# Kernel tuning notes

Measured on AMD Instinct MI355X. Metric: run time of the kernel, lower is better.

Reference implementation:

```python
import jax, jax.numpy as jnp
import numpy as np

# dims: S spaces, B batch, T tokens, D = dense_dim = concept_dim, K codebook size
S, B, T, D, K = 8, 8, 2048, 64, 512
BN_EPS = 1e-3  # keras BatchNormalization default


def setup_inputs() -> dict:
    key = jax.random.key(0)
    k0, k1, k2 = jax.random.split(key, 3)
    x = jax.random.normal(k0, (B, T, D), jnp.float32)
    W = jax.random.normal(k1, (S, D, D), jnp.float32) * 0.1   # per-space Dense kernels
    b = jnp.zeros((S, D), jnp.float32)                         # per-space Dense biases
    gamma = jnp.ones((S, D), jnp.float32)                      # BN scale
    beta = jnp.zeros((S, D), jnp.float32)                      # BN shift
    bn_mean = jnp.zeros((S, D), jnp.float32)                   # BN moving mean
    bn_var = jnp.ones((S, D), jnp.float32)                     # BN moving var
    E = jax.random.normal(k2, (S, K, D), jnp.float32)          # per-space codebooks
    return dict(x=x, W=W, b=b, gamma=gamma, beta=beta,
                bn_mean=bn_mean, bn_var=bn_var, E=E)


def reference(x, W, b, gamma, beta, bn_mean, bn_var, E):
    # per-space projection: Dense -> BatchNorm (inference) -> softmax gate
    proj = jnp.einsum('btd,sde->sbte', x, W) + b[:, None, None, :]          # [S,B,T,D]
    inv = jax.lax.rsqrt(bn_var + BN_EPS)
    bn = gamma[:, None, None, :] * (proj - bn_mean[:, None, None, :]) * inv[:, None, None, :] \
         + beta[:, None, None, :]
    att = jax.nn.softmax(bn, axis=-1)
    z = x[None] * att                                                       # z_e_att, [S,B,T,D]

    # squared euclidean distance to each code; argmin(norm) == argmin(dist^2)
    d2 = (jnp.sum(z * z, axis=-1, keepdims=True)
          - 2.0 * jnp.einsum('sbtc,skc->sbtk', z, E)
          + jnp.sum(E * E, axis=-1)[:, None, None, :])                      # [S,B,T,K]
    z_k = jnp.argmin(d2, axis=-1)                                           # [S,B,T] int

    # gather nearest codes per space, then add_n over spaces (set_att != 0)
    z_q_s = E[jnp.arange(S)[:, None, None], z_k]                            # [S,B,T,D]
    z_q = jnp.sum(z_q_s, axis=0)                                            # [B,T,D]
    z_e = jnp.sum(z, axis=0)                                                # [B,T,D]
    z_k = z_k.astype(jnp.int64) if z_k.dtype != jnp.int64 else z_k          # tf.argmin -> int64
    return z_q, z_e, z_k
```

## Files before the change

kernel.cpp:

```cpp
#include <hip/hip_runtime.h>
#include <cfloat>
#include <cmath>

#define SN 8
#define DN 64
#define KN 512
#define NN 16384
#define CK 64
#define REPAIR_THR 2e-3f
#define GAP_IK 8u
#define MAXFLAG 65536

#define WS_CNT 0
#define WS_SCL 16
#define WS_OFF (16 + SN*DN)
#define WS_E2  (WS_OFF + SN*DN)
#define WS_ENT (WS_E2 + SN*KN)
#define WS_WTH (WS_ENT + MAXFLAG)
#define WS_WTL (WS_WTH + SN*64*32)
#define WS_EH  (WS_WTL + SN*64*32)
#define WS_EL  (WS_EH + SN*KN*32)
#define WS_ZP  (WS_EL + SN*KN*32)
#define WS_END (WS_ZP + SN*NN*DN)

#define LDS_ZH 0
#define LDS_ZL 8192
#define LDS_EH 16384
#define LDS_EL 24576
#define LDS_TOTAL 32768

#define FB_LDS_R2    17408
#define FB_LDS_TAIL  33792
#define FB_LDS_TOTAL 34816

typedef __attribute__((ext_vector_type(8))) short bf16x8;
typedef __attribute__((ext_vector_type(4))) short s16x4;
typedef __attribute__((ext_vector_type(4))) float f32x4;

__device__ inline short bf_hi(float f, float& rem) {
    unsigned u = __float_as_uint(f);
    unsigned r = (u + 0x7fffu + ((u >> 16) & 1u)) & 0xffff0000u;
    rem = f - __uint_as_float(r);
    return (short)(r >> 16);
}
__device__ inline short bf_rn(float f) {
    unsigned u = __float_as_uint(f);
    return (short)((u + 0x7fffu + ((u >> 16) & 1u)) >> 16);
}
__device__ inline void cvt4(float a, float b, float c, float d, s16x4& h, s16x4& l) {
    float r0, r1, r2, r3;
    h.x = bf_hi(a, r0); h.y = bf_hi(b, r1); h.z = bf_hi(c, r2); h.w = bf_hi(d, r3);
    l.x = bf_rn(r0); l.y = bf_rn(r1); l.z = bf_rn(r2); l.w = bf_rn(r3);
}

union U8 { bf16x8 v; s16x4 q[2]; };

__global__ void prep_kernel(const float* __restrict__ b, const float* __restrict__ gamma,
                            const float* __restrict__ beta, const float* __restrict__ bmean,
                            const float* __restrict__ bvar, const float* __restrict__ E,
                            float* __restrict__ ws) {
    int tid = blockIdx.x * 256 + threadIdx.x;
    if (tid < SN * KN) {
        const float* er = E + (size_t)tid * DN;
        double a = 0.0;
        for (int d = 0; d < DN; ++d) { double v = (double)er[d]; a = fma(v, v, a); }
        ws[WS_E2 + tid] = (float)a;
    }
    int u = tid - SN * KN;
    if (u >= 0 && u < SN * DN) {
        double inv = 1.0 / sqrt((double)bvar[u] + 0.001);
        double sc  = (double)gamma[u] * inv;
        ws[WS_SCL + u] = (float)sc;
        ws[WS_OFF + u] = (float)(((double)b[u] - (double)bmean[u]) * sc + (double)beta[u]);
    }
}

__global__ void prep2_kernel(const float* __restrict__ E, float* __restrict__ ws) {
    int idx = blockIdx.x * 256 + threadIdx.x;
    int sk = idx >> 4, c4 = idx & 15;
    int k = sk & (KN - 1);
    float4 g = ((const float4*)E)[(size_t)sk * 16 + c4];
    s16x4 h4, l4;
    cvt4(g.x, g.y, g.z, g.w, h4, l4);
    size_t off = ((size_t)sk * 128 + c4 * 8) ^ ((k & 7) << 4);
    *(s16x4*)((char*)(ws + WS_EH) + off) = h4;
    *(s16x4*)((char*)(ws + WS_EL) + off) = l4;
}

__global__ void prep2w_kernel(const float* __restrict__ W, float* __restrict__ ws) {
    __shared__ float wt[64][65];
    int s = blockIdx.x;
    int tid = threadIdx.x;
    #pragma unroll
    for (int r = 0; r < 4; ++r) {
        int i = r * 256 + tid;
        float4 g = ((const float4*)W)[(size_t)s * 1024 + i];
        int d = i >> 4, c4 = i & 15;
        wt[d][c4 * 4 + 0] = g.x; wt[d][c4 * 4 + 1] = g.y;
        wt[d][c4 * 4 + 2] = g.z; wt[d][c4 * 4 + 3] = g.w;
    }
    __syncthreads();
    #pragma unroll
    for (int r = 0; r < 4; ++r) {
        int j = r * 256 + tid;
        int e = j >> 4, c4 = j & 15;
        s16x4 h4, l4;
        cvt4(wt[c4 * 4 + 0][e], wt[c4 * 4 + 1][e], wt[c4 * 4 + 2][e], wt[c4 * 4 + 3][e], h4, l4);
        size_t off = (size_t)(s * 64 + e) * 128 + c4 * 8;
        *(s16x4*)((char*)(ws + WS_WTH) + off) = h4;
        *(s16x4*)((char*)(ws + WS_WTL) + off) = l4;
    }
}

__launch_bounds__(256, 4)
__global__ void main_kernel(const float* __restrict__ x, float* __restrict__ ws,
                            float* __restrict__ out, int entcap) {
    extern __shared__ char smraw[];
    const int tid = threadIdx.x;
    const int s  = blockIdx.y;
    const int n0 = blockIdx.x * 64;
    const int lane = tid & 63;
    const int w    = tid >> 6;
    const int cc   = lane & 15;
    const int kq   = lane >> 4;
    const int arow = w * 16 + cc;
    const int axor = (arow & 7) << 4;

    const char* eimg_h = (const char*)(ws + WS_EH) + (size_t)s * KN * 128;
    const char* eimg_l = (const char*)(ws + WS_EL) + (size_t)s * KN * 128;

    float4 pf0 = *(const float4*)(eimg_h + tid * 16);
    float4 pf1 = *(const float4*)(eimg_h + 4096 + tid * 16);
    float4 pf2 = *(const float4*)(eimg_l + tid * 16);
    float4 pf3 = *(const float4*)(eimg_l + 4096 + tid * 16);

    U8 xah[2], xal[2];
    #pragma unroll
    for (int ks = 0; ks < 2; ++ks) {
        const float* xr = x + (size_t)(n0 + arow) * DN + ks * 32 + kq * 8;
        float4 a = *(const float4*)xr;
        float4 b2 = *(const float4*)(xr + 4);
        s16x4 h0, l0, h1, l1;
        cvt4(a.x, a.y, a.z, a.w, h0, l0);
        cvt4(b2.x, b2.y, b2.z, b2.w, h1, l1);
        xah[ks].q[0] = h0; xah[ks].q[1] = h1;
        xal[ks].q[0] = l0; xal[ks].q[1] = l1;
    }

    const char* wimg_h = (const char*)(ws + WS_WTH) + (size_t)s * 64 * 128;
    const char* wimg_l = (const char*)(ws + WS_WTL) + (size_t)s * 64 * 128;
    f32x4 pa[4];
    #pragma unroll
    for (int nt = 0; nt < 4; ++nt) pa[nt] = (f32x4){0.f, 0.f, 0.f, 0.f};
    #pragma unroll
    for (int ks = 0; ks < 2; ++ks) {
        #pragma unroll
        for (int nt = 0; nt < 4; ++nt) {
            int brow = nt * 16 + cc;
            bf16x8 bh = *(const bf16x8*)(wimg_h + brow * 128 + ks * 64 + kq * 16);
            bf16x8 bl = *(const bf16x8*)(wimg_l + brow * 128 + ks * 64 + kq * 16);
            pa[nt] = __builtin_amdgcn_mfma_f32_16x16x32_bf16(xah[ks].v, bh, pa[nt], 0, 0, 0);
            pa[nt] = __builtin_amdgcn_mfma_f32_16x16x32_bf16(xah[ks].v, bl, pa[nt], 0, 0, 0);
            pa[nt] = __builtin_amdgcn_mfma_f32_16x16x32_bf16(xal[ks].v, bh, pa[nt], 0, 0, 0);
        }
    }

    float sclv[4], oflv[4];
    #pragma unroll
    for (int nt = 0; nt < 4; ++nt) {
        sclv[nt] = ws[WS_SCL + s * 64 + nt * 16 + cc];
        oflv[nt] = ws[WS_OFF + s * 64 + nt * 16 + cc];
    }
    float zzq[4];
    #pragma unroll
    for (int r = 0; r < 4; ++r) {
        int t = w * 16 + kq * 4 + r;
        float v0 = fmaf(pa[0][r], sclv[0], oflv[0]);
        float v1 = fmaf(pa[1][r], sclv[1], oflv[1]);
        float v2 = fmaf(pa[2][r], sclv[2], oflv[2]);
        float v3 = fmaf(pa[3][r], sclv[3], oflv[3]);
        float mx = fmaxf(fmaxf(v0, v1), fmaxf(v2, v3));
        mx = fmaxf(mx, __shfl_xor(mx, 1)); mx = fmaxf(mx, __shfl_xor(mx, 2));
        mx = fmaxf(mx, __shfl_xor(mx, 4)); mx = fmaxf(mx, __shfl_xor(mx, 8));
        float e0 = expf(v0 - mx), e1 = expf(v1 - mx), e2v = expf(v2 - mx), e3 = expf(v3 - mx);
        float sm = e0 + e1 + e2v + e3;
        sm += __shfl_xor(sm, 1); sm += __shfl_xor(sm, 2);
        sm += __shfl_xor(sm, 4); sm += __shfl_xor(sm, 8);
        float inv = 1.0f / sm;
        float att[4] = { e0 * inv, e1 * inv, e2v * inv, e3 * inv };
        float zz = 0.f;
        int txor = (t & 7) << 4;
        #pragma unroll
        for (int nt = 0; nt < 4; ++nt) {
            int e = nt * 16 + cc;
            float xv = x[(size_t)(n0 + t) * DN + e];
            float z = xv * att[nt];
            zz += z * z;
            float rem; short zh = bf_hi(z, rem); short zl = bf_rn(rem);
            int zoff = (t * 128 + e * 2) ^ txor;
            *(short*)(smraw + LDS_ZH + zoff) = zh;
            *(short*)(smraw + LDS_ZL + zoff) = zl;
            ws[WS_ZP + ((size_t)s * NN + n0 + t) * DN + e] = z;
        }
        zz += __shfl_xor(zz, 1); zz += __shfl_xor(zz, 2);
        zz += __shfl_xor(zz, 4); zz += __shfl_xor(zz, 8);
        zzq[r] = (zz + 16.f) * 4096.f;
    }
    *(float4*)(smraw + LDS_EH + tid * 16) = pf0;
    *(float4*)(smraw + LDS_EH + 4096 + tid * 16) = pf1;
    *(float4*)(smraw + LDS_EL + tid * 16) = pf2;
    *(float4*)(smraw + LDS_EL + 4096 + tid * 16) = pf3;
    __syncthreads();

    unsigned m1[4], m2[4];
    #pragma unroll
    for (int r = 0; r < 4; ++r) { m1[r] = 0xFFFFFFFFu; m2[r] = 0xFFFFFFFFu; }

    for (int kk = 0; kk < KN; kk += CK) {
        if (kk + CK < KN) {
            const char* nbh = eimg_h + (size_t)(kk + CK) * 128;
            const char* nbl = eimg_l + (size_t)(kk + CK) * 128;
            pf0 = *(const float4*)(nbh + tid * 16);
            pf1 = *(const float4*)(nbh + 4096 + tid * 16);
            pf2 = *(const float4*)(nbl + tid * 16);
            pf3 = *(const float4*)(nbl + 4096 + tid * 16);
        }
        float e2v[4];
        #pragma unroll
        for (int nt = 0; nt < 4; ++nt) e2v[nt] = ws[WS_E2 + s * KN + kk + nt * 16 + cc];

        bf16x8 zah[2], zal[2];
        #pragma unroll
        for (int ks = 0; ks < 2; ++ks) {
            int aoff = (arow * 128 + kq * 16 + ks * 64) ^ axor;
            zah[ks] = *(const bf16x8*)(smraw + LDS_ZH + aoff);
            zal[ks] = *(const bf16x8*)(smraw + LDS_ZL + aoff);
        }
        f32x4 acc[4];
        #pragma unroll
        for (int nt = 0; nt < 4; ++nt) acc[nt] = (f32x4){0.f, 0.f, 0.f, 0.f};
        #pragma unroll
        for (int ks = 0; ks < 2; ++ks) {
            #pragma unroll
            for (int nt = 0; nt < 4; ++nt) {
                int brow = nt * 16 + cc;
                int boff = (brow * 128 + kq * 16 + ks * 64) ^ ((brow & 7) << 4);
                bf16x8 bh = *(const bf16x8*)(smraw + LDS_EH + boff);
                bf16x8 bl = *(const bf16x8*)(smraw + LDS_EL + boff);
                acc[nt] = __builtin_amdgcn_mfma_f32_16x16x32_bf16(zah[ks], bh, acc[nt], 0, 0, 0);
                acc[nt] = __builtin_amdgcn_mfma_f32_16x16x32_bf16(zah[ks], bl, acc[nt], 0, 0, 0);
                acc[nt] = __builtin_amdgcn_mfma_f32_16x16x32_bf16(zal[ks], bh, acc[nt], 0, 0, 0);
            }
        }
        #pragma unroll
        for (int nt = 0; nt < 4; ++nt) {
            unsigned kx = (unsigned)(kk + nt * 16 + cc);
            float eb = fmaf(4096.f, e2v[nt], 0.f);
            #pragma unroll
            for (int r = 0; r < 4; ++r) {
                float cell = fmaf(-8192.f, acc[nt][r], zzq[r] + eb);
                float dc = fminf(cell, 4194300.f);
                unsigned key = (((unsigned)dc) << 9) | kx;
                m2[r] = min(m2[r], max(m1[r], key));
                m1[r] = min(m1[r], key);
            }
        }
        if (kk + CK < KN) {
            __syncthreads();
            *(float4*)(smraw + LDS_EH + tid * 16) = pf0;
            *(float4*)(smraw + LDS_EH + 4096 + tid * 16) = pf1;
            *(float4*)(smraw + LDS_EL + tid * 16) = pf2;
            *(float4*)(smraw + LDS_EL + 4096 + tid * 16) = pf3;
            __syncthreads();
        }
    }

    #pragma unroll
    for (int mask = 1; mask <= 8; mask <<= 1) {
        #pragma unroll
        for (int r = 0; r < 4; ++r) {
            unsigned o1 = (unsigned)__shfl_xor((int)m1[r], mask);
            unsigned o2 = (unsigned)__shfl_xor((int)m2[r], mask);
            unsigned hi = max(m1[r], o1);
            m1[r] = min(m1[r], o1);
            m2[r] = min(min(m2[r], o2), hi);
        }
    }
    #pragma unroll
    for (int r = 0; r < 4; ++r) {
        int n = n0 + w * 16 + kq * 4 + r;
        if (cc == 0) {
            int k1 = (int)(m1[r] & 511u);
            out[2 * NN * DN + s * NN + n] = (float)k1;
            if ((m2[r] >> 9) - (m1[r] >> 9) <= GAP_IK) {
                int idx = atomicAdd((int*)ws, 1);
                if (idx < entcap) ((int*)ws)[WS_ENT + idx] = (s << 14) | n;
            }
        }
    }
}

__launch_bounds__(256, 4)
__global__ void main_fb_kernel(const float* __restrict__ x, const float* __restrict__ W,
                               const float* __restrict__ E, float* __restrict__ ws,
                               float* __restrict__ out, int entcap) {
    extern __shared__ char smraw[];
    float4* xs4 = (float4*)smraw;
    float4* ws4 = (float4*)(smraw + FB_LDS_R2);
    char* ehb = smraw;
    char* elb = smraw + 8192;
    char* zhb = smraw + FB_LDS_R2;
    char* zlb = smraw + FB_LDS_R2 + 8192;
    float* tailf = (float*)(smraw + FB_LDS_TAIL);
    float* e2s = tailf; float* scl = tailf + 64; float* ofl = tailf + 128; float* zzs = tailf + 192;

    const int tid = threadIdx.x;
    const int tg = tid >> 4, lg = tid & 15;
    const int s  = blockIdx.y;
    const int n0 = blockIdx.x * 64;
    const float4* xg4 = (const float4*)x;
    const float4* Wg4 = (const float4*)W;
    const float4* Eg4 = (const float4*)E;

    #pragma unroll
    for (int r = 0; r < 4; ++r) {
        int i = r * 256 + tid;
        xs4[(i >> 4) * 17 + (i & 15)] = xg4[n0 * 16 + i];
        ws4[i] = Wg4[s * 1024 + i];
    }
    if (tid < 64) { scl[tid] = ws[WS_SCL + s * 64 + tid]; ofl[tid] = ws[WS_OFF + s * 64 + tid]; }
    __syncthreads();

    float pa[4][4];
    #pragma unroll
    for (int ti = 0; ti < 4; ++ti)
        #pragma unroll
        for (int j = 0; j < 4; ++j) pa[ti][j] = 0.f;
    #pragma unroll 4
    for (int c = 0; c < 16; ++c) {
        float4 xv[4], wv[4];
        #pragma unroll
        for (int ti = 0; ti < 4; ++ti) xv[ti] = xs4[(tg * 4 + ti) * 17 + c];
        #pragma unroll
        for (int dd = 0; dd < 4; ++dd) wv[dd] = ws4[(c * 4 + dd) * 16 + lg];
        #pragma unroll
        for (int ti = 0; ti < 4; ++ti) {
            float a0 = pa[ti][0], a1 = pa[ti][1], a2 = pa[ti][2], a3 = pa[ti][3];
            a0 = fmaf(xv[ti].x, wv[0].x, a0); a0 = fmaf(xv[ti].y, wv[1].x, a0);
            a0 = fmaf(xv[ti].z, wv[2].x, a0); a0 = fmaf(xv[ti].w, wv[3].x, a0);
            a1 = fmaf(xv[ti].x, wv[0].y, a1); a1 = fmaf(xv[ti].y, wv[1].y, a1);
            a1 = fmaf(xv[ti].z, wv[2].y, a1); a1 = fmaf(xv[ti].w, wv[3].y, a1);
            a2 = fmaf(xv[ti].x, wv[0].z, a2); a2 = fmaf(xv[ti].y, wv[1].z, a2);
            a2 = fmaf(xv[ti].z, wv[2].z, a2); a2 = fmaf(xv[ti].w, wv[3].z, a2);
            a3 = fmaf(xv[ti].x, wv[0].w, a3); a3 = fmaf(xv[ti].y, wv[1].w, a3);
            a3 = fmaf(xv[ti].z, wv[2].w, a3); a3 = fmaf(xv[ti].w, wv[3].w, a3);
            pa[ti][0] = a0; pa[ti][1] = a1; pa[ti][2] = a2; pa[ti][3] = a3;
        }
    }
    __syncthreads();

    {
        float s0 = scl[lg * 4 + 0], s1 = scl[lg * 4 + 1], s2 = scl[lg * 4 + 2], s3 = scl[lg * 4 + 3];
        float o0 = ofl[lg * 4 + 0], o1 = ofl[lg * 4 + 1], o2 = ofl[lg * 4 + 2], o3 = ofl[lg * 4 + 3];
        #pragma unroll
        for (int ti = 0; ti < 4; ++ti) {
            int t = tg * 4 + ti;
            float v0 = fmaf(pa[ti][0], s0, o0);
            float v1 = fmaf(pa[ti][1], s1, o1);
            float v2 = fmaf(pa[ti][2], s2, o2);
            float v3 = fmaf(pa[ti][3], s3, o3);
            float mx = fmaxf(fmaxf(v0, v1), fmaxf(v2, v3));
            mx = fmaxf(mx, __shfl_xor(mx, 1)); mx = fmaxf(mx, __shfl_xor(mx, 2));
            mx = fmaxf(mx, __shfl_xor(mx, 4)); mx = fmaxf(mx, __shfl_xor(mx, 8));
            float e0 = expf(v0 - mx), e1 = expf(v1 - mx), e2v = expf(v2 - mx), e3 = expf(v3 - mx);
            float sm = e0 + e1 + e2v + e3;
            sm += __shfl_xor(sm, 1); sm += __shfl_xor(sm, 2);
            sm += __shfl_xor(sm, 4); sm += __shfl_xor(sm, 8);
            float inv = 1.0f / sm;
            float4 xv = xs4[t * 17 + lg];
            float z0 = xv.x * (e0 * inv), z1 = xv.y * (e1 * inv);
            float z2 = xv.z * (e2v * inv), z3 = xv.w * (e3 * inv);
            float zz = z0 * z0 + z1 * z1 + z2 * z2 + z3 * z3;
            zz += __shfl_xor(zz, 1); zz += __shfl_xor(zz, 2);
            zz += __shfl_xor(zz, 4); zz += __shfl_xor(zz, 8);
            if (lg == 0) zzs[t] = zz;
            s16x4 h4, l4;
            cvt4(z0, z1, z2, z3, h4, l4);
            int zoff = (t * 128 + lg * 8) ^ ((t & 7) << 4);
            *(s16x4*)(zhb + zoff) = h4;
            *(s16x4*)(zlb + zoff) = l4;
            float* pz = out + NN * DN + (size_t)(n0 + t) * DN + lg * 4;
            atomicAdd(pz + 0, z0); atomicAdd(pz + 1, z1);
            atomicAdd(pz + 2, z2); atomicAdd(pz + 3, z3);
        }
    }
    __syncthreads();

    const int lane = tid & 63;
    const int w    = tid >> 6;
    const int arow = w * 16 + (lane & 15);
    const int kg16 = (lane >> 4) * 16;
    const int axor = (arow & 7) << 4;
    const int abase = arow * 128 + kg16;

    float zzv[4];
    #pragma unroll
    for (int r = 0; r < 4; ++r) zzv[r] = zzs[w * 16 + (lane >> 4) * 4 + r];

    float m1[4], m2[4]; int k1[4];
    #pragma unroll
    for (int r = 0; r < 4; ++r) { m1[r] = FLT_MAX; m2[r] = FLT_MAX; k1[r] = 0x7fffffff; }

    for (int kk = 0; kk < KN; kk += CK) {
        __syncthreads();
        #pragma unroll
        for (int r = 0; r < 4; ++r) {
            int i = r * 256 + tid;
            float4 g = Eg4[(s * KN + kk) * 16 + i];
            int row = i >> 4, c4 = i & 15;
            s16x4 h4, l4;
            cvt4(g.x, g.y, g.z, g.w, h4, l4);
            int off = (row * 128 + c4 * 8) ^ ((row & 7) << 4);
            *(s16x4*)(ehb + off) = h4;
            *(s16x4*)(elb + off) = l4;
        }
        if (tid < 64) e2s[tid] = ws[WS_E2 + s * KN + kk + tid];
        __syncthreads();

        f32x4 acc[4];
        #pragma unroll
        for (int nt = 0; nt < 4; ++nt) acc[nt] = (f32x4){0.f, 0.f, 0.f, 0.f};
        #pragma unroll
        for (int ks = 0; ks < 2; ++ks) {
            int aoff = (abase + ks * 64) ^ axor;
            bf16x8 ah = *(const bf16x8*)(zhb + aoff);
            bf16x8 al = *(const bf16x8*)(zlb + aoff);
            #pragma unroll
            for (int nt = 0; nt < 4; ++nt) {
                int brow = nt * 16 + (lane & 15);
                int boff = (brow * 128 + kg16 + ks * 64) ^ ((brow & 7) << 4);
                bf16x8 bh = *(const bf16x8*)(ehb + boff);
                bf16x8 bl = *(const bf16x8*)(elb + boff);
                acc[nt] = __builtin_amdgcn_mfma_f32_16x16x32_bf16(ah, bh, acc[nt], 0, 0, 0);
                acc[nt] = __builtin_amdgcn_mfma_f32_16x16x32_bf16(ah, bl, acc[nt], 0, 0, 0);
                acc[nt] = __builtin_amdgcn_mfma_f32_16x16x32_bf16(al, bh, acc[nt], 0, 0, 0);
            }
        }
        #pragma unroll
        for (int nt = 0; nt < 4; ++nt) {
            float e2v = e2s[nt * 16 + (lane & 15)];
            int kx = kk + nt * 16 + (lane & 15);
            #pragma unroll
            for (int r = 0; r < 4; ++r) {
                float d2 = fmaf(-2.0f, acc[nt][r], zzv[r]) + e2v;
                if (d2 < m1[r]) { m2[r] = m1[r]; m1[r] = d2; k1[r] = kx; }
                else if (d2 < m2[r]) { m2[r] = d2; }
            }
        }
    }

    #pragma unroll
    for (int mask = 1; mask <= 8; mask <<= 1) {
        #pragma unroll
        for (int r = 0; r < 4; ++r) {
            float om1 = __shfl_xor(m1[r], mask);
            int   ok1 = __shfl_xor(k1[r], mask);
            float om2 = __shfl_xor(m2[r], mask);
            bool better = (om1 < m1[r]) || (om1 == m1[r] && ok1 < k1[r]);
            float nm2 = better ? fminf(m1[r], om2) : fminf(om1, m2[r]);
            if (better) { m1[r] = om1; k1[r] = ok1; }
            m2[r] = nm2;
        }
    }
    #pragma unroll
    for (int r = 0; r < 4; ++r) {
        int t = w * 16 + (lane >> 4) * 4 + r;
        int n = n0 + t;
        if ((lane & 15) == 0) {
            out[2 * NN * DN + s * NN + n] = (float)k1[r];
            if (m2[r] - m1[r] < REPAIR_THR) {
                int idx = atomicAdd((int*)ws, 1);
                if (idx < entcap) ((int*)ws)[WS_ENT + idx] = (s << 14) | n;
            }
        }
        int kb = __shfl(k1[r], lane & 48);
        float4 eg = Eg4[(s * KN + kb) * 16 + (lane & 15)];
        float* q = out + (size_t)n * DN + (lane & 15) * 4;
        atomicAdd(q + 0, eg.x); atomicAdd(q + 1, eg.y);
        atomicAdd(q + 2, eg.z); atomicAdd(q + 3, eg.w);
    }
}

__global__ void reduce_kernel(const float* __restrict__ E, const float* __restrict__ ws,
                              float* __restrict__ out) {
    int idx = blockIdx.x * 256 + threadIdx.x;
    int n = idx >> 4, c = idx & 15;
    const float4* zp4 = (const float4*)(ws + WS_ZP);
    float4 ze = make_float4(0.f, 0.f, 0.f, 0.f);
    #pragma unroll
    for (int s = 0; s < SN; ++s) {
        float4 v = zp4[((size_t)s * NN + n) * 16 + c];
        ze.x += v.x; ze.y += v.y; ze.z += v.z; ze.w += v.w;
    }
    ((float4*)out)[NN * 16 + (size_t)n * 16 + c] = ze;

    float4 zq = make_float4(0.f, 0.f, 0.f, 0.f);
    #pragma unroll
    for (int s = 0; s < SN; ++s) {
        int k = (int)(out[2 * NN * DN + s * NN + n] + 0.5f);
        float4 e = ((const float4*)E)[((size_t)s * KN + k) * 16 + c];
        zq.x += e.x; zq.y += e.y; zq.z += e.z; zq.w += e.w;
    }
    ((float4*)out)[(size_t)n * 16 + c] = zq;
}

__global__ void repair_kernel(const float* __restrict__ x, const float* __restrict__ W,
                              const float* __restrict__ b, const float* __restrict__ gamma,
                              const float* __restrict__ beta, const float* __restrict__ bmean,
                              const float* __restrict__ bvar, const float* __restrict__ E,
                              float* __restrict__ ws, float* __restrict__ out, int entcap) {
    __shared__ double zd[64];
    __shared__ double red[256];
    __shared__ int redk[256];
    __shared__ double zzsh;
    __shared__ int shk[2];
    int cnt = ((int*)ws)[0]; if (cnt > entcap) cnt = entcap;
    const int tid = threadIdx.x;
    for (int idx = blockIdx.x; idx < cnt; idx += gridDim.x) {
        int code = ((int*)ws)[WS_ENT + idx];
        int s = code >> 14, n = code & (NN - 1);
        int e = tid & 63, q = tid >> 6;
        const float* xrow = x + (size_t)n * 64;
        double p0 = 0.0, p1 = 0.0, p2 = 0.0, p3 = 0.0;
        for (int d = q * 16; d < q * 16 + 16; d += 4) {
            p0 = fma((double)xrow[d],     (double)W[((size_t)s * 64 + d) * 64 + e],     p0);
            p1 = fma((double)xrow[d + 1], (double)W[((size_t)s * 64 + d + 1) * 64 + e], p1);
            p2 = fma((double)xrow[d + 2], (double)W[((size_t)s * 64 + d + 2) * 64 + e], p2);
            p3 = fma((double)xrow[d + 3], (double)W[((size_t)s * 64 + d + 3) * 64 + e], p3);
        }
        red[tid] = (p0 + p1) + (p2 + p3);
        __syncthreads();
        if (tid < 64) {
            double proj = (red[tid] + red[tid + 64]) + (red[tid + 128] + red[tid + 192]);
            double inv = 1.0 / sqrt((double)bvar[s * 64 + e] + 0.001);
            double bn = (double)gamma[s * 64 + e] * ((proj + (double)b[s * 64 + e]) - (double)bmean[s * 64 + e]) * inv
                      + (double)beta[s * 64 + e];
            double m = bn;
            #pragma unroll
            for (int mask = 1; mask <= 32; mask <<= 1) m = fmax(m, __shfl_xor(m, mask));
            double ex = exp(bn - m);
            double sm = ex;
            #pragma unroll
            for (int mask = 1; mask <= 32; mask <<= 1) sm += __shfl_xor(sm, mask);
            double z = (double)xrow[e] * (ex / sm);
            zd[e] = z;
            double zz = z * z;
            #pragma unroll
            for (int mask = 1; mask <= 32; mask <<= 1) zz += __shfl_xor(zz, mask);
            if (tid == 0) zzsh = zz;
        }
        __syncthreads();
        double bv = DBL_MAX; int bk = 1 << 30;
        for (int k = tid; k < KN; k += 256) {
            const float* er = E + ((size_t)s * KN + k) * 64;
            double d0 = 0.0, d1 = 0.0, d2a = 0.0, d3 = 0.0;
            double f0 = 0.0, f1 = 0.0, f2 = 0.0, f3 = 0.0;
            for (int d = 0; d < 64; d += 4) {
                double e0 = (double)er[d], e1 = (double)er[d + 1];
                double e2d = (double)er[d + 2], e3d = (double)er[d + 3];
                d0 = fma(zd[d], e0, d0);     d1 = fma(zd[d + 1], e1, d1);
                d2a = fma(zd[d + 2], e2d, d2a); d3 = fma(zd[d + 3], e3d, d3);
                f0 = fma(e0, e0, f0); f1 = fma(e1, e1, f1);
                f2 = fma(e2d, e2d, f2); f3 = fma(e3d, e3d, f3);
            }
            double dot = (d0 + d1) + (d2a + d3);
            double e2t = (f0 + f1) + (f2 + f3);
            double d2v = (zzsh - 2.0 * dot) + e2t;
            if (d2v < bv) { bv = d2v; bk = k; }
        }
        #pragma unroll
        for (int mask = 1; mask <= 32; mask <<= 1) {
            double ov = __shfl_xor(bv, mask);
            int   ok = __shfl_xor(bk, mask);
            if (ov < bv || (ov == bv && ok < bk)) { bv = ov; bk = ok; }
        }
        if ((tid & 63) == 0) { red[tid >> 6] = bv; redk[tid >> 6] = bk; }
        __syncthreads();
        if (tid == 0) {
            double m = red[0]; int mk = redk[0];
            for (int i = 1; i < 4; ++i)
                if (red[i] < m || (red[i] == m && redk[i] < mk)) { m = red[i]; mk = redk[i]; }
            int kold = (int)(out[2 * NN * 64 + s * NN + n] + 0.5f);
            shk[0] = mk; shk[1] = kold;
            out[2 * NN * 64 + s * NN + n] = (float)mk;
        }
        __syncthreads();
        int mk = shk[0], kold = shk[1];
        if (mk != kold && tid < 64)
            atomicAdd(out + n * 64 + tid, E[((size_t)s * KN + mk) * 64 + tid] - E[((size_t)s * KN + kold) * 64 + tid]);
        __syncthreads();
    }
}

extern "C" void kernel_launch(void* const* d_in, const int* in_sizes, int n_in,
                              void* d_out, int out_size, void* d_ws, size_t ws_size,
                              hipStream_t stream) {
    const float* x     = (const float*)d_in[0];
    const float* W     = (const float*)d_in[1];
    const float* b     = (const float*)d_in[2];
    const float* gamma = (const float*)d_in[3];
    const float* beta  = (const float*)d_in[4];
    const float* bmean = (const float*)d_in[5];
    const float* bvar  = (const float*)d_in[6];
    const float* E     = (const float*)d_in[7];
    float* out = (float*)d_out;
    float* ws  = (float*)d_ws;

    bool staged = ws_size >= (size_t)WS_END * 4;

    long avail = (long)(ws_size / 4) - WS_ENT - 16;
    if (avail < 0) avail = 0;
    int entcap = (int)(avail > MAXFLAG ? MAXFLAG : avail);
    if (staged) entcap = MAXFLAG;

    hipMemsetAsync(d_ws, 0, 64, stream);
    prep_kernel<<<18, 256, 0, stream>>>(b, gamma, beta, bmean, bvar, E, ws);
    dim3 grid(256, 8);
    if (staged) {
        prep2w_kernel<<<8, 256, 0, stream>>>(W, ws);
        prep2_kernel<<<256, 256, 0, stream>>>(E, ws);
        main_kernel<<<grid, 256, LDS_TOTAL, stream>>>(x, ws, out, entcap);
        reduce_kernel<<<1024, 256, 0, stream>>>(E, ws, out);
    } else {
        hipMemsetAsync(d_out, 0, (size_t)(2 * NN * DN) * sizeof(float), stream);
        main_fb_kernel<<<grid, 256, FB_LDS_TOTAL, stream>>>(x, W, E, ws, out, entcap);
    }
    repair_kernel<<<2048, 256, 0, stream>>>(x, W, b, gamma, beta, bmean, bvar, E, ws, out, entcap);
}
```

Before: 158.5 us.

## Merge prep kernels, double-buffer codebook LDS tiles, hoist z fragments

Folds the three preprocessing kernels into one launch and precomputes the scaled codebook norms so the inner loop does one fewer multiply. Double-buffers the codebook tiles in shared memory, which cuts the two barriers per chunk down to one. It also hoists the z-fragment LDS loads out of the loop, switches to fast exp, and drops the clamp on the distance key. The cost is more LDS per block (occupancy bound lowered from 4 to 3) and a smaller repair-flag capacity. The missing clamp and the fast exp could shift which argmin candidates get flagged for repair.

New measurement: 153.0 us. 3.5% less time.

```diff
diff --git a/kernel.cpp b/kernel.cpp
--- a/kernel.cpp
+++ b/kernel.cpp
@@ -9,7 +9,7 @@
 #define CK 64
 #define REPAIR_THR 2e-3f
 #define GAP_IK 8u
-#define MAXFLAG 65536
+#define MAXFLAG 32768
 
 #define WS_CNT 0
 #define WS_SCL 16
@@ -21,13 +21,13 @@
 #define WS_EH  (WS_WTL + SN*64*32)
 #define WS_EL  (WS_EH + SN*KN*32)
 #define WS_ZP  (WS_EL + SN*KN*32)
-#define WS_END (WS_ZP + SN*NN*DN)
+#define WS_E2S (WS_ZP + SN*NN*DN)
+#define WS_END (WS_E2S + SN*KN)
 
 #define LDS_ZH 0
 #define LDS_ZL 8192
-#define LDS_EH 16384
-#define LDS_EL 24576
-#define LDS_TOTAL 32768
+#define LDS_E0 16384
+#define LDS_TOTAL 49152
 
 #define FB_LDS_R2    17408
 #define FB_LDS_TAIL  33792
@@ -54,6 +54,62 @@
 }
 
 union U8 { bf16x8 v; s16x4 q[2]; };
+
+__global__ void prep_all_kernel(const float* __restrict__ b, const float* __restrict__ gamma,
+                                const float* __restrict__ beta, const float* __restrict__ bmean,
+                                const float* __restrict__ bvar, const float* __restrict__ W,
+                                const float* __restrict__ E, float* __restrict__ ws) {
+    __shared__ float wt[64][65];
+    const int blk = blockIdx.x, tid = threadIdx.x;
+    if (blk < 256) {
+        int idx = blk * 256 + tid;
+        int sk = idx >> 4, c4 = idx & 15;
+        int k = sk & (KN - 1);
+        float4 g = ((const float4*)E)[(size_t)sk * 16 + c4];
+        s16x4 h4, l4;
+        cvt4(g.x, g.y, g.z, g.w, h4, l4);
+        size_t off = ((size_t)sk * 128 + c4 * 8) ^ ((k & 7) << 4);
+        *(s16x4*)((char*)(ws + WS_EH) + off) = h4;
+        *(s16x4*)((char*)(ws + WS_EL) + off) = l4;
+    } else if (blk < 264) {
+        int s = blk - 256;
+        #pragma unroll
+        for (int r = 0; r < 4; ++r) {
+            int i = r * 256 + tid;
+            float4 g = ((const float4*)W)[(size_t)s * 1024 + i];
+            int d = i >> 4, c4 = i & 15;
+            wt[d][c4 * 4 + 0] = g.x; wt[d][c4 * 4 + 1] = g.y;
+            wt[d][c4 * 4 + 2] = g.z; wt[d][c4 * 4 + 3] = g.w;
+        }
+        __syncthreads();
+        #pragma unroll
+        for (int r = 0; r < 4; ++r) {
+            int j = r * 256 + tid;
+            int e = j >> 4, c4 = j & 15;
+            s16x4 h4, l4;
+            cvt4(wt[c4 * 4 + 0][e], wt[c4 * 4 + 1][e], wt[c4 * 4 + 2][e], wt[c4 * 4 + 3][e], h4, l4);
+            size_t off = (size_t)(s * 64 + e) * 128 + c4 * 8;
+            *(s16x4*)((char*)(ws + WS_WTH) + off) = h4;
+            *(s16x4*)((char*)(ws + WS_WTL) + off) = l4;
+        }
+    } else {
+        int t2 = (blk - 264) * 256 + tid;
+        if (t2 < SN * KN) {
+            const float* er = E + (size_t)t2 * DN;
+            double a = 0.0;
+            for (int d = 0; d < DN; ++d) { double v = (double)er[d]; a = fma(v, v, a); }
+            ws[WS_E2 + t2]  = (float)a;
+            ws[WS_E2S + t2] = (float)(a * 4096.0);
+        }
+        int u = t2 - SN * KN;
+        if (u >= 0 && u < SN * DN) {
+            double inv = 1.0 / sqrt((double)bvar[u] + 0.001);
+            double sc  = (double)gamma[u] * inv;
+            ws[WS_SCL + u] = (float)sc;
+            ws[WS_OFF + u] = (float)(((double)b[u] - (double)bmean[u]) * sc + (double)beta[u]);
+        }
+    }
+}
 
 __global__ void prep_kernel(const float* __restrict__ b, const float* __restrict__ gamma,
                             const float* __restrict__ beta, const float* __restrict__ bmean,
@@ -75,44 +131,7 @@
     }
 }
 
-__global__ void prep2_kernel(const float* __restrict__ E, float* __restrict__ ws) {
-    int idx = blockIdx.x * 256 + threadIdx.x;
-    int sk = idx >> 4, c4 = idx & 15;
-    int k = sk & (KN - 1);
-    float4 g = ((const float4*)E)[(size_t)sk * 16 + c4];
-    s16x4 h4, l4;
-    cvt4(g.x, g.y, g.z, g.w, h4, l4);
-    size_t off = ((size_t)sk * 128 + c4 * 8) ^ ((k & 7) << 4);
-    *(s16x4*)((char*)(ws + WS_EH) + off) = h4;
-    *(s16x4*)((char*)(ws + WS_EL) + off) = l4;
-}
-
-__global__ void prep2w_kernel(const float* __restrict__ W, float* __restrict__ ws) {
-    __shared__ float wt[64][65];
-    int s = blockIdx.x;
-    int tid = threadIdx.x;
-    #pragma unroll
-    for (int r = 0; r < 4; ++r) {
-        int i = r * 256 + tid;
-        float4 g = ((const float4*)W)[(size_t)s * 1024 + i];
-        int d = i >> 4, c4 = i & 15;
-        wt[d][c4 * 4 + 0] = g.x; wt[d][c4 * 4 + 1] = g.y;
-        wt[d][c4 * 4 + 2] = g.z; wt[d][c4 * 4 + 3] = g.w;
-    }
-    __syncthreads();
-    #pragma unroll
-    for (int r = 0; r < 4; ++r) {
-        int j = r * 256 + tid;
-        int e = j >> 4, c4 = j & 15;
-        s16x4 h4, l4;
-        cvt4(wt[c4 * 4 + 0][e], wt[c4 * 4 + 1][e], wt[c4 * 4 + 2][e], wt[c4 * 4 + 3][e], h4, l4);
-        size_t off = (size_t)(s * 64 + e) * 128 + c4 * 8;
-        *(s16x4*)((char*)(ws + WS_WTH) + off) = h4;
-        *(s16x4*)((char*)(ws + WS_WTL) + off) = l4;
-    }
-}
-
-__launch_bounds__(256, 4)
+__launch_bounds__(256, 3)
 __global__ void main_kernel(const float* __restrict__ x, float* __restrict__ ws,
                             float* __restrict__ out, int entcap) {
     extern __shared__ char smraw[];
@@ -182,7 +201,8 @@
         float mx = fmaxf(fmaxf(v0, v1), fmaxf(v2, v3));
         mx = fmaxf(mx, __shfl_xor(mx, 1)); mx = fmaxf(mx, __shfl_xor(mx, 2));
         mx = fmaxf(mx, __shfl_xor(mx, 4)); mx = fmaxf(mx, __shfl_xor(mx, 8));
-        float e0 = expf(v0 - mx), e1 = expf(v1 - mx), e2v = expf(v2 - mx), e3 = expf(v3 - mx);
+        float e0 = __expf(v0 - mx), e1 = __expf(v1 - mx);
+        float e2v = __expf(v2 - mx), e3 = __expf(v3 - mx);
         float sm = e0 + e1 + e2v + e3;
         sm += __shfl_xor(sm, 1); sm += __shfl_xor(sm, 2);
         sm += __shfl_xor(sm, 4); sm += __shfl_xor(sm, 8);
@@ -206,18 +226,31 @@
         zz += __shfl_xor(zz, 4); zz += __shfl_xor(zz, 8);
         zzq[r] = (zz + 16.f) * 4096.f;
     }
-    *(float4*)(smraw + LDS_EH + tid * 16) = pf0;
-    *(float4*)(smraw + LDS_EH + 4096 + tid * 16) = pf1;
-    *(float4*)(smraw + LDS_EL + tid * 16) = pf2;
-    *(float4*)(smraw + LDS_EL + 4096 + tid * 16) = pf3;
-    __syncthreads();
+
+    bf16x8 zah[2], zal[2];
+    #pragma unroll
+    for (int ks = 0; ks < 2; ++ks) {
+        int aoff = (arow * 128 + kq * 16 + ks * 64) ^ axor;
+        zah[ks] = *(const bf16x8*)(smraw + LDS_ZH + aoff);
+        zal[ks] = *(const bf16x8*)(smraw + LDS_ZL + aoff);
+    }
 
     unsigned m1[4], m2[4];
     #pragma unroll
     for (int r = 0; r < 4; ++r) { m1[r] = 0xFFFFFFFFu; m2[r] = 0xFFFFFFFFu; }
 
-    for (int kk = 0; kk < KN; kk += CK) {
-        if (kk + CK < KN) {
+    int p = 0;
+    #pragma unroll 1
+    for (int c = 0; c < KN / CK; ++c) {
+        char* ebuf = smraw + LDS_E0 + p * 16384;
+        *(float4*)(ebuf + tid * 16) = pf0;
+        *(float4*)(ebuf + 4096 + tid * 16) = pf1;
+        *(float4*)(ebuf + 8192 + tid * 16) = pf2;
+        *(float4*)(ebuf + 12288 + tid * 16) = pf3;
+        __syncthreads();
+
+        int kk = c * CK;
+        if (c < KN / CK - 1) {
             const char* nbh = eimg_h + (size_t)(kk + CK) * 128;
             const char* nbl = eimg_l + (size_t)(kk + CK) * 128;
             pf0 = *(const float4*)(nbh + tid * 16);
@@ -227,15 +260,8 @@
         }
         float e2v[4];
         #pragma unroll
-        for (int nt = 0; nt < 4; ++nt) e2v[nt] = ws[WS_E2 + s * KN + kk + nt * 16 + cc];
-
-        bf16x8 zah[2], zal[2];
-        #pragma unroll
-        for (int ks = 0; ks < 2; ++ks) {
-            int aoff = (arow * 128 + kq * 16 + ks * 64) ^ axor;
-            zah[ks] = *(const bf16x8*)(smraw + LDS_ZH + aoff);
-            zal[ks] = *(const bf16x8*)(smraw + LDS_ZL + aoff);
-        }
+        for (int nt = 0; nt < 4; ++nt) e2v[nt] = ws[WS_E2S + s * KN + kk + nt * 16 + cc];
+
         f32x4 acc[4];
         #pragma unroll
         for (int nt = 0; nt < 4; ++nt) acc[nt] = (f32x4){0.f, 0.f, 0.f, 0.f};
@@ -245,8 +271,8 @@
             for (int nt = 0; nt < 4; ++nt) {
                 int brow = nt * 16 + cc;
                 int boff = (brow * 128 + kq * 16 + ks * 64) ^ ((brow & 7) << 4);
-                bf16x8 bh = *(const bf16x8*)(smraw + LDS_EH + boff);
-                bf16x8 bl = *(const bf16x8*)(smraw + LDS_EL + boff);
+                bf16x8 bh = *(const bf16x8*)(ebuf + boff);
+                bf16x8 bl = *(const bf16x8*)(ebuf + 8192 + boff);
                 acc[nt] = __builtin_amdgcn_mfma_f32_16x16x32_bf16(zah[ks], bh, acc[nt], 0, 0, 0);
                 acc[nt] = __builtin_amdgcn_mfma_f32_16x16x32_bf16(zah[ks], bl, acc[nt], 0, 0, 0);
                 acc[nt] = __builtin_amdgcn_mfma_f32_16x16x32_bf16(zal[ks], bh, acc[nt], 0, 0, 0);
@@ -255,24 +281,15 @@
         #pragma unroll
         for (int nt = 0; nt < 4; ++nt) {
             unsigned kx = (unsigned)(kk + nt * 16 + cc);
-            float eb = fmaf(4096.f, e2v[nt], 0.f);
             #pragma unroll
             for (int r = 0; r < 4; ++r) {
-                float cell = fmaf(-8192.f, acc[nt][r], zzq[r] + eb);
-                float dc = fminf(cell, 4194300.f);
-                unsigned key = (((unsigned)dc) << 9) | kx;
+                float cell = fmaf(-8192.f, acc[nt][r], zzq[r] + e2v[nt]);
+                unsigned key = (((unsigned)cell) << 9) | kx;
                 m2[r] = min(m2[r], max(m1[r], key));
                 m1[r] = min(m1[r], key);
             }
         }
-        if (kk + CK < KN) {
-            __syncthreads();
-            *(float4*)(smraw + LDS_EH + tid * 16) = pf0;
-            *(float4*)(smraw + LDS_EH + 4096 + tid * 16) = pf1;
-            *(float4*)(smraw + LDS_EL + tid * 16) = pf2;
-            *(float4*)(smraw + LDS_EL + 4096 + tid * 16) = pf3;
-            __syncthreads();
-        }
+        p ^= 1;
     }
 
     #pragma unroll
@@ -624,14 +641,13 @@
     if (staged) entcap = MAXFLAG;
 
     hipMemsetAsync(d_ws, 0, 64, stream);
-    prep_kernel<<<18, 256, 0, stream>>>(b, gamma, beta, bmean, bvar, E, ws);
     dim3 grid(256, 8);
     if (staged) {
-        prep2w_kernel<<<8, 256, 0, stream>>>(W, ws);
-        prep2_kernel<<<256, 256, 0, stream>>>(E, ws);
+        prep_all_kernel<<<282, 256, 0, stream>>>(b, gamma, beta, bmean, bvar, W, E, ws);
         main_kernel<<<grid, 256, LDS_TOTAL, stream>>>(x, ws, out, entcap);
         reduce_kernel<<<1024, 256, 0, stream>>>(E, ws, out);
     } else {
+        prep_kernel<<<18, 256, 0, stream>>>(b, gamma, beta, bmean, bvar, E, ws);
         hipMemsetAsync(d_out, 0, (size_t)(2 * NN * DN) * sizeof(float), stream);
         main_fb_kernel<<<grid, 256, FB_LDS_TOTAL, stream>>>(x, W, E, ws, out, entcap);
     }
```
